# Kernel optimization log

Hardware: AMD Instinct MI355X
Metric: run time of the kernel (lower is better)

## Reference

```python
import jax, jax.numpy as jnp
import numpy as np

B, T_ENC, T_DEC, D, N_STATE = 32, 1024, 512, 512, 512


def setup_inputs() -> dict:
    key = jax.random.key(0)
    k1, k2, k3, k4 = jax.random.split(key, 4)
    scale = 1.0 / np.sqrt(D)
    return {
        "states_encoder": jax.random.normal(k1, (B, T_ENC, D), dtype=jnp.float32),
        "states_decoder": jax.random.normal(k2, (B, T_DEC, N_STATE), dtype=jnp.float32),
        "Wk": jax.random.normal(k3, (D, N_STATE), dtype=jnp.float32) * scale,
        "bk": jnp.zeros((N_STATE,), dtype=jnp.float32),
        "Wv": jax.random.normal(k4, (D, N_STATE), dtype=jnp.float32) * scale,
        "bv": jnp.zeros((N_STATE,), dtype=jnp.float32),
    }


def reference(states_encoder, states_decoder, Wk, bk, Wv, bv):
    # general Luong dot-product attention (n_state = int branch)
    key_vector = states_encoder @ Wk + bk          # [B, T_enc, N]
    val_vector = states_encoder @ Wv + bv          # [B, T_enc, N]
    # score[b, t_dec, t_enc] = sum_n dec[b,t_dec,n] * key[b,t_enc,n]
    score = jnp.einsum('bqn,bkn->bqk', states_decoder, key_vector)
    attention = jax.nn.softmax(score, axis=-1)     # over encoder positions
    # context[b, t_dec, n] = sum_k attention[b,t_dec,k] * val[b,k,n]
    context = jnp.einsum('bqk,bkn->bqn', attention, val_vector)
    return (context, attention)
```

## Files before the change

### kernel.cpp

```cpp
#include <hip/hip_runtime.h>
#include <math.h>

#define BB    32
#define TENC  1024
#define TDEC  512
#define DDIM  512
#define NST   512

typedef _Float16 f16_t;
typedef _Float16 f16x8 __attribute__((ext_vector_type(8)));
typedef _Float16 f16x4 __attribute__((ext_vector_type(4)));
typedef float    f32x4 __attribute__((ext_vector_type(4)));

#define GLOAD_LDS16(gp, lp) __builtin_amdgcn_global_load_lds( \
    (const __attribute__((address_space(1))) unsigned int*)(const void*)(gp), \
    (__attribute__((address_space(3))) unsigned int*)(lp), 16, 0, 0)

static __device__ __forceinline__ f32x4 MFMA16H(f16x8 a, f16x8 b, f32x4 c) {
    return __builtin_amdgcn_mfma_f32_16x16x32_f16(a, b, c, 0, 0, 0);
}

__global__ __launch_bounds__(256)
void prep_convert(const float* __restrict__ enc, const float* __restrict__ Wk,
                  const float* __restrict__ Wv,
                  f16_t* __restrict__ Ef16, f16_t* __restrict__ Wk16,
                  f16_t* __restrict__ WvT16)
{
    const int bid = blockIdx.x;
    const int t = threadIdx.x;

    if (bid < 8320) {
        const float* src; f16_t* dst; long i;
        if (bid < 8192) { src = enc; dst = Ef16; i = (long)bid * 256 + t; }
        else            { src = Wk;  dst = Wk16; i = (long)(bid - 8192) * 256 + t; }
        float4 a = *(const float4*)&src[i * 8];
        float4 b = *(const float4*)&src[i * 8 + 4];
        f16x8 o;
        o[0] = (f16_t)a.x; o[1] = (f16_t)a.y; o[2] = (f16_t)a.z; o[3] = (f16_t)a.w;
        o[4] = (f16_t)b.x; o[5] = (f16_t)b.y; o[6] = (f16_t)b.z; o[7] = (f16_t)b.w;
        *(f16x8*)&dst[i * 8] = o;
        return;
    }

    __shared__ f16_t tile[64][65];
    const int r2 = bid - 8320;
    const int c0 = (r2 & 7) * 64, r0 = (r2 >> 3) * 64;
    const int rr = t >> 4;
    const int cc = (t & 15) * 4;
#pragma unroll
    for (int p = 0; p < 4; ++p) {
        int r = rr + p * 16;
        float4 v = *(const float4*)&Wv[(long)(r0 + r) * NST + c0 + cc];
        tile[r][cc + 0] = (f16_t)v.x;
        tile[r][cc + 1] = (f16_t)v.y;
        tile[r][cc + 2] = (f16_t)v.z;
        tile[r][cc + 3] = (f16_t)v.w;
    }
    __syncthreads();
    const int dr = t >> 2;
    const int tc = (t & 3) * 16;
    f16_t tmp[16];
#pragma unroll
    for (int e = 0; e < 16; ++e) tmp[e] = tile[tc + e][dr];
    *(f16x8*)&WvT16[(long)(c0 + dr) * DDIM + r0 + tc]     = *(f16x8*)&tmp[0];
    *(f16x8*)&WvT16[(long)(c0 + dr) * DDIM + r0 + tc + 8] = *(f16x8*)&tmp[8];
}

__global__ __launch_bounds__(256)
void transpose_f16(const f16_t* __restrict__ in, f16_t* __restrict__ out,
                   int R, int C, long sIn, long sOut)
{
    __shared__ f16_t tile[64][65];
    const long b = blockIdx.z;
    in  += b * sIn;
    out += b * sOut;
    const int r0 = blockIdx.x * 64;
    const int c0 = blockIdx.y * 64;
    const int t = threadIdx.x;
    const int rr = t >> 4;
    const int cc = (t & 15) * 4;
#pragma unroll
    for (int p = 0; p < 4; ++p) {
        const int r = rr + p * 16;
        *(f16x4*)&tile[r][cc] = *(const f16x4*)&in[(long)(r0 + r) * C + c0 + cc];
    }
    __syncthreads();
    const int dr = t >> 2;
    const int tc = (t & 3) * 16;
    f16_t tmp[16];
#pragma unroll
    for (int e = 0; e < 16; ++e) tmp[e] = tile[tc + e][dr];
    *(f16x8*)&out[(long)(c0 + dr) * R + r0 + tc]     = *(f16x8*)&tmp[0];
    *(f16x8*)&out[(long)(c0 + dr) * R + r0 + tc + 8] = *(f16x8*)&tmp[8];
}

template<int EPI>
__global__ __launch_bounds__(256)
void gemm_h(const f16_t* __restrict__ A, const f16_t* __restrict__ B,
            void* __restrict__ C0,
            int M, int N, int K, long sA, long sB, long sC)
{
    __shared__ f16_t lds[2][8192];

    const int tid  = threadIdx.x;
    const int wave = tid >> 6;
    const int lane = tid & 63;

    const int gx = gridDim.x, gy = gridDim.y;
    const long nwg = (long)gx * gy * gridDim.z;
    const long fo  = ((long)blockIdx.z * gy + blockIdx.y) * gx + blockIdx.x;
    const long f2 = (fo & 7) * (nwg >> 3) + (fo >> 3);
    const int bx  = (int)(f2 % gx);
    const int by  = (int)((f2 / gx) % gy);
    const long bz = f2 / ((long)gx * gy);

    const f16_t* Ab = A + bz * sA;
    const f16_t* Bb = B + bz * sB;

    const int row0 = by * 128;
    const int col0 = bx * 128;

    const int srow  = wave * 16 + (lane >> 2);
    const int sslot = (lane & 3) ^ ((srow >> 1) & 3);
    const int wdst  = wave * 512;
    const long aOff0 = (long)(row0 + srow) * K + sslot * 8;
    const long aOff1 = (long)(row0 + 64 + srow) * K + sslot * 8;
    const long bOff0 = (long)(col0 + srow) * K + sslot * 8;
    const long bOff1 = (long)(col0 + 64 + srow) * K + sslot * 8;

    const int fr = lane & 15;
    const int q  = lane >> 4;
    const int wr = (wave >> 1) * 64;
    const int wc = (wave & 1) * 64;
    int aro[4], bro[4];
#pragma unroll
    for (int i = 0; i < 4; ++i) {
        const int r = wr + i * 16 + fr;
        aro[i] = r * 32 + ((q ^ ((r >> 1) & 3)) * 8);
    }
#pragma unroll
    for (int j = 0; j < 4; ++j) {
        const int r = wc + j * 16 + fr;
        bro[j] = r * 32 + ((q ^ ((r >> 1) & 3)) * 8);
    }

    f32x4 acc[4][4] = {};
    const int NT = K >> 5;

#define STAGE(buf, kt) do {                                   \
        GLOAD_LDS16(Ab + aOff0 + (kt), &(buf)[wdst]);         \
        GLOAD_LDS16(Ab + aOff1 + (kt), &(buf)[2048 + wdst]);  \
        GLOAD_LDS16(Bb + bOff0 + (kt), &(buf)[4096 + wdst]);  \
        GLOAD_LDS16(Bb + bOff1 + (kt), &(buf)[6144 + wdst]);  \
    } while (0)

    STAGE(lds[0], 0);

    for (int t = 0; t < NT; ++t) {
        const f16_t* cur = lds[t & 1];
        f16_t* nxt = lds[(t & 1) ^ 1];
        const bool pf = (t + 1 < NT);

        __builtin_amdgcn_sched_barrier(0);
        __builtin_amdgcn_s_barrier();
        if (pf) {
            STAGE(nxt, (t + 1) << 5);
            asm volatile("s_waitcnt vmcnt(4)" ::: "memory");
        } else {
            asm volatile("s_waitcnt vmcnt(0)" ::: "memory");
        }
        __builtin_amdgcn_s_barrier();
        __builtin_amdgcn_sched_barrier(0);

        f16x8 aH[4], bH[4];
#pragma unroll
        for (int i = 0; i < 4; ++i) aH[i] = *(const f16x8*)&cur[aro[i]];
#pragma unroll
        for (int j = 0; j < 4; ++j) bH[j] = *(const f16x8*)&cur[4096 + bro[j]];

#pragma unroll
        for (int j = 0; j < 4; ++j)
#pragma unroll
            for (int i = 0; i < 4; ++i)
                acc[i][j] = MFMA16H(aH[i], bH[j], acc[i][j]);
    }
#undef STAGE

    const int frow = q * 4;
#pragma unroll
    for (int i = 0; i < 4; ++i) {
        const int rgl = row0 + wr + i * 16 + frow;
#pragma unroll
        for (int j = 0; j < 4; ++j) {
            const int cg = col0 + wc + j * 16 + fr;
            if constexpr (EPI == 2) {
                f16_t* C = (f16_t*)C0 + bz * sC;
#pragma unroll
                for (int r = 0; r < 4; ++r)
                    C[(long)(rgl + r) * N + cg] = (f16_t)acc[i][j][r];
            } else {
                float* C = (float*)C0 + bz * sC;
#pragma unroll
                for (int r = 0; r < 4; ++r)
                    C[(long)(rgl + r) * N + cg] = acc[i][j][r];
            }
        }
    }
}

template<int EPI>
__global__ __launch_bounds__(256)
void gemm_rs(const float* __restrict__ Rf, const f16_t* __restrict__ Gh,
             const float* __restrict__ bias, void* __restrict__ C0,
             int M, int N, int K, long sRf, long sG, long sC)
{
    __shared__ f16_t lds[2][8192];

    const int tid  = threadIdx.x;
    const int wave = tid >> 6;
    const int lane = tid & 63;

    const int gx = gridDim.x, gy = gridDim.y;
    const long nwg = (long)gx * gy * gridDim.z;
    const long fo  = ((long)blockIdx.z * gy + blockIdx.y) * gx + blockIdx.x;
    const long f2 = (fo & 7) * (nwg >> 3) + (fo >> 3);
    const int bx  = (int)(f2 % gx);
    const int by  = (int)((f2 / gx) % gy);
    const long bz = f2 / ((long)gx * gy);

    const float* RfB = Rf + bz * sRf;
    const f16_t* GhB = Gh + bz * sG;

    const int row0 = by * 128;
    const int col0 = bx * 128;

    const int srow  = wave * 16 + (lane >> 2);
    const int sslot = (lane & 3) ^ ((srow >> 1) & 3);
    const int wdst  = wave * 512;

    const int rrow = tid >> 3;
    const int rk4  = (tid & 7) * 4;
    const int rgr  = rk4 >> 3;
    const int rh4  = rk4 & 4;

    const int fr = lane & 15;
    const int q  = lane >> 4;
    const int wr = (wave >> 1) * 64;
    const int wc = (wave & 1) * 64;
    int aro[4], bro[4];
#pragma unroll
    for (int i = 0; i < 4; ++i) {
        const int r = wr + i * 16 + fr;
        aro[i] = r * 32 + ((q ^ ((r >> 1) & 3)) * 8);
    }
#pragma unroll
    for (int j = 0; j < 4; ++j) {
        const int r = wc + j * 16 + fr;
        bro[j] = r * 32 + ((q ^ ((r >> 1) & 3)) * 8);
    }

    f32x4 acc[4][4] = {};
    float4 rS[4];
    f16x8 aH[4], bH[4];
    const int NT = K >> 5;

    auto stageG = [&](f16_t* buf, int kt) {
#pragma unroll
        for (int c = 0; c < 2; ++c) {
            const long go = (long)(col0 + c * 64 + srow) * K + kt + sslot * 8;
            GLOAD_LDS16(GhB + go, &buf[4096 + c * 2048 + wdst]);
        }
    };
    auto loadR = [&](int kt) {
#pragma unroll
        for (int i = 0; i < 4; ++i)
            rS[i] = *(const float4*)&RfB[(long)(row0 + i * 32 + rrow) * K + kt + rk4];
    };
    auto writeR = [&](f16_t* buf) {
#pragma unroll
        for (int i = 0; i < 4; ++i) {
            const int row = i * 32 + rrow;
            const int eo  = row * 32 + ((rgr ^ ((row >> 1) & 3)) * 8) + rh4;
            f16x4 h4;
            h4[0] = (f16_t)rS[i].x; h4[1] = (f16_t)rS[i].y;
            h4[2] = (f16_t)rS[i].z; h4[3] = (f16_t)rS[i].w;
            *(f16x4*)&buf[eo] = h4;
        }
    };
    auto readF = [&](const f16_t* buf) {
#pragma unroll
        for (int i = 0; i < 4; ++i) aH[i] = *(const f16x8*)&buf[aro[i]];
#pragma unroll
        for (int j = 0; j < 4; ++j) bH[j] = *(const f16x8*)&buf[4096 + bro[j]];
    };

    loadR(0);
    stageG(lds[0], 0);
    writeR(lds[0]);
    loadR(32);
    asm volatile("s_waitcnt vmcnt(4)" ::: "memory");
    asm volatile("s_waitcnt lgkmcnt(0)" ::: "memory");
    __builtin_amdgcn_s_barrier();
    readF(lds[0]);
    asm volatile("s_waitcnt lgkmcnt(0)" ::: "memory");
    __builtin_amdgcn_s_barrier();

    for (int t = 0; t < NT; ++t) {
        f16_t* nxt = lds[(t & 1) ^ 1];
        const bool pf = (t + 1 < NT);

        if (pf) {
            writeR(nxt);
            stageG(nxt, (t + 1) << 5);
            if (t + 2 < NT) loadR((t + 2) << 5);
        }
#pragma unroll
        for (int j = 0; j < 4; ++j)
#pragma unroll
            for (int i = 0; i < 4; ++i)
                acc[i][j] = MFMA16H(aH[i], bH[j], acc[i][j]);

        if (pf && (t + 2 < NT))
            asm volatile("s_waitcnt vmcnt(4)" ::: "memory");
        else
            asm volatile("s_waitcnt vmcnt(0)" ::: "memory");
        asm volatile("s_waitcnt lgkmcnt(0)" ::: "memory");
        __builtin_amdgcn_s_barrier();
        if (pf) {
            readF(nxt);
            asm volatile("s_waitcnt lgkmcnt(0)" ::: "memory");
        }
        __builtin_amdgcn_s_barrier();
    }

    const int frow = q * 4;
#pragma unroll
    for (int i = 0; i < 4; ++i) {
        const int rgl = row0 + wr + i * 16 + frow;
#pragma unroll
        for (int j = 0; j < 4; ++j) {
            const int cg = col0 + wc + j * 16 + fr;
            if constexpr (EPI == 2) {
                f16_t* C = (f16_t*)C0 + bz * sC;
#pragma unroll
                for (int r = 0; r < 4; ++r)
                    C[(long)(rgl + r) * N + cg] = (f16_t)acc[i][j][r];
            } else {
                float* C = (float*)C0 + bz * sC;
                const float badd = bias[cg];
#pragma unroll
                for (int r = 0; r < 4; ++r)
                    C[(long)(rgl + r) * N + cg] = acc[i][j][r] + badd;
            }
        }
    }
}

__global__ __launch_bounds__(256)
void softmax_rows(float* __restrict__ S)
{
    const long row = (long)blockIdx.x * 4 + (threadIdx.x >> 6);
    const int lane = threadIdx.x & 63;
    float* p = S + row * (long)TENC;

    float4 v[4];
    float m = -INFINITY;
#pragma unroll
    for (int i = 0; i < 4; ++i) {
        v[i] = *(const float4*)&p[i * 256 + lane * 4];
        m = fmaxf(fmaxf(fmaxf(v[i].x, v[i].y), fmaxf(v[i].z, v[i].w)), m);
    }
#pragma unroll
    for (int o = 32; o; o >>= 1) m = fmaxf(m, __shfl_xor(m, o, 64));

    float s = 0.f;
#pragma unroll
    for (int i = 0; i < 4; ++i) {
        v[i].x = __expf(v[i].x - m);
        v[i].y = __expf(v[i].y - m);
        v[i].z = __expf(v[i].z - m);
        v[i].w = __expf(v[i].w - m);
        s += v[i].x + v[i].y + v[i].z + v[i].w;
    }
#pragma unroll
    for (int o = 32; o; o >>= 1) s += __shfl_xor(s, o, 64);

    const float inv = 1.0f / s;
#pragma unroll
    for (int i = 0; i < 4; ++i) {
        v[i].x *= inv; v[i].y *= inv; v[i].z *= inv; v[i].w *= inv;
        *(float4*)&p[i * 256 + lane * 4] = v[i];
    }
}

#define TILE_M 64
#define TILE_N 64
#define TILE_K 16
template<bool B_TRANS, bool ADD_BIAS>
__global__ __launch_bounds__(256)
void gemm_f32(const float* __restrict__ A, const float* __restrict__ Bm,
              const float* __restrict__ bias, float* __restrict__ C,
              int M, int N, int K, int lda, int ldb,
              long strideA, long strideB, long strideC)
{
    __shared__ float As[TILE_K][TILE_M + 4];
    __shared__ float Bs[TILE_K][TILE_N + 4];
    const int b = blockIdx.z;
    A += (long)b * strideA; Bm += (long)b * strideB; C += (long)b * strideC;
    const int tid = threadIdx.x;
    const int tx = tid & 15, ty = tid >> 4;
    const int row0 = blockIdx.y * TILE_M, col0 = blockIdx.x * TILE_N;
    const int am = tid >> 2, ak = (tid & 3) * 4;
    float acc[4][4] = {};
    for (int kt = 0; kt < K; kt += TILE_K) {
        float4 a4 = *(const float4*)&A[(long)(row0 + am) * lda + kt + ak];
        float4 b4;
        if (B_TRANS) b4 = *(const float4*)&Bm[(long)(col0 + am) * ldb + kt + ak];
        else {
            const int bk_ = tid >> 4, bn = (tid & 15) * 4;
            b4 = *(const float4*)&Bm[(long)(kt + bk_) * ldb + col0 + bn];
        }
        __syncthreads();
        As[ak + 0][am] = a4.x; As[ak + 1][am] = a4.y;
        As[ak + 2][am] = a4.z; As[ak + 3][am] = a4.w;
        if (B_TRANS) {
            Bs[ak + 0][am] = b4.x; Bs[ak + 1][am] = b4.y;
            Bs[ak + 2][am] = b4.z; Bs[ak + 3][am] = b4.w;
        } else {
            const int bk_ = tid >> 4, bn = (tid & 15) * 4;
            *(float4*)&Bs[bk_][bn] = b4;
        }
        __syncthreads();
#pragma unroll
        for (int k = 0; k < TILE_K; ++k) {
            float4 av = *(const float4*)&As[k][ty * 4];
            float4 bv4 = *(const float4*)&Bs[k][tx * 4];
            float ar[4] = {av.x, av.y, av.z, av.w};
            float br[4] = {bv4.x, bv4.y, bv4.z, bv4.w};
#pragma unroll
            for (int i = 0; i < 4; ++i)
#pragma unroll
                for (int j = 0; j < 4; ++j)
                    acc[i][j] = fmaf(ar[i], br[j], acc[i][j]);
        }
    }
    float4 bias4 = make_float4(0.f, 0.f, 0.f, 0.f);
    if (ADD_BIAS) bias4 = *(const float4*)&bias[col0 + tx * 4];
#pragma unroll
    for (int i = 0; i < 4; ++i) {
        float4 o;
        o.x = acc[i][0] + bias4.x; o.y = acc[i][1] + bias4.y;
        o.z = acc[i][2] + bias4.z; o.w = acc[i][3] + bias4.w;
        *(float4*)&C[(long)(row0 + ty * 4 + i) * N + col0 + tx * 4] = o;
    }
}

extern "C" void kernel_launch(void* const* d_in, const int* in_sizes, int n_in,
                              void* d_out, int out_size, void* d_ws, size_t ws_size,
                              hipStream_t stream)
{
    const float* enc = (const float*)d_in[0];
    const float* dec = (const float*)d_in[1];
    const float* Wk  = (const float*)d_in[2];
    const float* Wv  = (const float*)d_in[4];
    const float* bv  = (const float*)d_in[5];

    const long nD = (long)BB * TDEC * NST;

    float* ctx   = (float*)d_out;
    float* attnF = ctx + nD;

    const size_t need = 68157440;
    const dim3 blk(256);

    if (ws_size < need) {
        float* ws = (float*)d_ws;
        gemm_f32<true, false><<<dim3(DDIM / 64, (BB * TDEC) / 64, 1), blk, 0, stream>>>(
            dec, Wk, nullptr, ws, BB * TDEC, DDIM, NST, NST, NST, 0, 0, 0);
        gemm_f32<true, false><<<dim3(TENC / 64, TDEC / 64, BB), blk, 0, stream>>>(
            ws, enc, nullptr, attnF, TDEC, TENC, DDIM, DDIM, DDIM,
            (long)TDEC * DDIM, (long)TENC * DDIM, (long)TDEC * TENC);
        softmax_rows<<<(BB * TDEC) / 4, blk, 0, stream>>>(attnF);
        gemm_f32<false, false><<<dim3(DDIM / 64, TDEC / 64, BB), blk, 0, stream>>>(
            attnF, enc, nullptr, ws, TDEC, DDIM, TENC, TENC, DDIM,
            (long)TDEC * TENC, (long)TENC * DDIM, (long)TDEC * DDIM);
        gemm_f32<false, true><<<dim3(NST / 64, (BB * TDEC) / 64, 1), blk, 0, stream>>>(
            ws, Wv, bv, ctx, BB * TDEC, NST, DDIM, DDIM, NST, 0, 0, 0);
        return;
    }

    char* w = (char*)d_ws;
    f16_t* EVT   = (f16_t*)(w);
    f16_t* Ef16  = (f16_t*)(w + 33554432);
    f16_t* Wk16  = (f16_t*)(w + 67108864);
    f16_t* WvT16 = (f16_t*)(w + 67633152);

    f16_t* DK16 = (f16_t*)ctx;
    f16_t* EV   = (f16_t*)attnF;

    prep_convert<<<8384, blk, 0, stream>>>(enc, Wk, Wv, Ef16, Wk16, WvT16);

    gemm_rs<2><<<dim3(DDIM / 128, (BB * TDEC) / 128, 1), blk, 0, stream>>>(
        dec, Wk16, nullptr, DK16,
        BB * TDEC, DDIM, NST, 0, 0, 0);

    gemm_h<2><<<dim3(NST / 128, (BB * TENC) / 128, 1), blk, 0, stream>>>(
        Ef16, WvT16, EV,
        BB * TENC, NST, DDIM, 0, 0, 0);

    transpose_f16<<<dim3(TENC / 64, NST / 64, BB), blk, 0, stream>>>(
        EV, EVT, TENC, NST, (long)TENC * NST, (long)NST * TENC);

    gemm_h<0><<<dim3(TENC / 128, TDEC / 128, BB), blk, 0, stream>>>(
        DK16, Ef16, attnF,
        TDEC, TENC, DDIM,
        (long)TDEC * DDIM, (long)TENC * DDIM, (long)TDEC * TENC);

    softmax_rows<<<(BB * TDEC) / 4, blk, 0, stream>>>(attnF);

    gemm_rs<3><<<dim3(NST / 128, TDEC / 128, BB), blk, 0, stream>>>(
        attnF, EVT, bv, ctx,
        TDEC, NST, TENC,
        (long)TDEC * TENC, (long)NST * TENC, (long)TDEC * NST);
}
```

Baseline: 173.5 us.

## Reassociate value projection after attention and read fp32 encoder directly in score GEMM

Instead of projecting encoder states through Wv and transposing the result, the pipeline now computes attention @ encoder and applies Wv (plus bias) afterwards on the smaller decoder-length output. The score GEMM reads the fp32 encoder directly through a register-staged path with a new AREG template switch, which removes the separate fp16 encoder conversion. A single fused convert-and-transpose of the encoder feeds the attention-times-encoder GEMM. This reduces total FLOPs and intermediate traffic because T_DEC is smaller than T_ENC. The cost is extra fp32 loads and in-kernel conversion in the score GEMM, plus an fp16 intermediate before the final projection.

```diff
diff --git a/kernel.cpp b/kernel.cpp
--- a/kernel.cpp
+++ b/kernel.cpp
@@ -21,29 +21,25 @@
 }
 
 __global__ __launch_bounds__(256)
-void prep_convert(const float* __restrict__ enc, const float* __restrict__ Wk,
-                  const float* __restrict__ Wv,
-                  f16_t* __restrict__ Ef16, f16_t* __restrict__ Wk16,
-                  f16_t* __restrict__ WvT16)
+void prep_weights(const float* __restrict__ Wk, const float* __restrict__ Wv,
+                  f16_t* __restrict__ Wk16, f16_t* __restrict__ WvT16)
 {
     const int bid = blockIdx.x;
     const int t = threadIdx.x;
 
-    if (bid < 8320) {
-        const float* src; f16_t* dst; long i;
-        if (bid < 8192) { src = enc; dst = Ef16; i = (long)bid * 256 + t; }
-        else            { src = Wk;  dst = Wk16; i = (long)(bid - 8192) * 256 + t; }
-        float4 a = *(const float4*)&src[i * 8];
-        float4 b = *(const float4*)&src[i * 8 + 4];
+    if (bid < 128) {
+        long i = (long)bid * 256 + t;
+        float4 a = *(const float4*)&Wk[i * 8];
+        float4 b = *(const float4*)&Wk[i * 8 + 4];
         f16x8 o;
         o[0] = (f16_t)a.x; o[1] = (f16_t)a.y; o[2] = (f16_t)a.z; o[3] = (f16_t)a.w;
         o[4] = (f16_t)b.x; o[5] = (f16_t)b.y; o[6] = (f16_t)b.z; o[7] = (f16_t)b.w;
-        *(f16x8*)&dst[i * 8] = o;
+        *(f16x8*)&Wk16[i * 8] = o;
         return;
     }
 
     __shared__ f16_t tile[64][65];
-    const int r2 = bid - 8320;
+    const int r2 = bid - 128;
     const int c0 = (r2 & 7) * 64, r0 = (r2 >> 3) * 64;
     const int rr = t >> 4;
     const int cc = (t & 15) * 4;
@@ -67,22 +63,25 @@
 }
 
 __global__ __launch_bounds__(256)
-void transpose_f16(const f16_t* __restrict__ in, f16_t* __restrict__ out,
-                   int R, int C, long sIn, long sOut)
+void transpose_ef(const float* __restrict__ in, f16_t* __restrict__ out)
 {
     __shared__ f16_t tile[64][65];
     const long b = blockIdx.z;
-    in  += b * sIn;
-    out += b * sOut;
-    const int r0 = blockIdx.x * 64;
-    const int c0 = blockIdx.y * 64;
+    const float* inB = in + b * (long)TENC * DDIM;
+    f16_t* outB = out + b * (long)DDIM * TENC;
+    const int te0 = blockIdx.x * 64;
+    const int d0  = blockIdx.y * 64;
     const int t = threadIdx.x;
     const int rr = t >> 4;
     const int cc = (t & 15) * 4;
 #pragma unroll
     for (int p = 0; p < 4; ++p) {
         const int r = rr + p * 16;
-        *(f16x4*)&tile[r][cc] = *(const f16x4*)&in[(long)(r0 + r) * C + c0 + cc];
+        float4 v = *(const float4*)&inB[(long)(te0 + r) * DDIM + d0 + cc];
+        tile[r][cc + 0] = (f16_t)v.x;
+        tile[r][cc + 1] = (f16_t)v.y;
+        tile[r][cc + 2] = (f16_t)v.z;
+        tile[r][cc + 3] = (f16_t)v.w;
     }
     __syncthreads();
     const int dr = t >> 2;
@@ -90,15 +89,15 @@
     f16_t tmp[16];
 #pragma unroll
     for (int e = 0; e < 16; ++e) tmp[e] = tile[tc + e][dr];
-    *(f16x8*)&out[(long)(c0 + dr) * R + r0 + tc]     = *(f16x8*)&tmp[0];
-    *(f16x8*)&out[(long)(c0 + dr) * R + r0 + tc + 8] = *(f16x8*)&tmp[8];
-}
-
-template<int EPI>
+    *(f16x8*)&outB[(long)(d0 + dr) * TENC + te0 + tc]     = *(f16x8*)&tmp[0];
+    *(f16x8*)&outB[(long)(d0 + dr) * TENC + te0 + tc + 8] = *(f16x8*)&tmp[8];
+}
+
+template<int AREG, int EPI>
 __global__ __launch_bounds__(256)
-void gemm_h(const f16_t* __restrict__ A, const f16_t* __restrict__ B,
-            void* __restrict__ C0,
-            int M, int N, int K, long sA, long sB, long sC)
+void gemm_rs(const float* __restrict__ Rf, const f16_t* __restrict__ Gh,
+             const float* __restrict__ bias, void* __restrict__ C0,
+             int M, int N, int K, long sRf, long sG, long sC)
 {
     __shared__ f16_t lds[2][8192];
 
@@ -114,19 +113,24 @@
     const int by  = (int)((f2 / gx) % gy);
     const long bz = f2 / ((long)gx * gy);
 
-    const f16_t* Ab = A + bz * sA;
-    const f16_t* Bb = B + bz * sB;
+    const float* RfB = Rf + bz * sRf;
+    const f16_t* GhB = Gh + bz * sG;
 
     const int row0 = by * 128;
     const int col0 = bx * 128;
+    const int rbase = AREG ? row0 : col0;
+    const int gbase = AREG ? col0 : row0;
+    constexpr int rOff = AREG ? 0 : 4096;
+    constexpr int gOff = AREG ? 4096 : 0;
 
     const int srow  = wave * 16 + (lane >> 2);
     const int sslot = (lane & 3) ^ ((srow >> 1) & 3);
     const int wdst  = wave * 512;
-    const long aOff0 = (long)(row0 + srow) * K + sslot * 8;
-    const long aOff1 = (long)(row0 + 64 + srow) * K + sslot * 8;
-    const long bOff0 = (long)(col0 + srow) * K + sslot * 8;
-    const long bOff1 = (long)(col0 + 64 + srow) * K + sslot * 8;
+
+    const int rrow = tid >> 3;
+    const int rk4  = (tid & 7) * 4;
+    const int rgr  = rk4 >> 3;
+    const int rh4  = rk4 & 4;
 
     const int fr = lane & 15;
     const int q  = lane >> 4;
@@ -145,121 +149,6 @@
     }
 
     f32x4 acc[4][4] = {};
-    const int NT = K >> 5;
-
-#define STAGE(buf, kt) do {                                   \
-        GLOAD_LDS16(Ab + aOff0 + (kt), &(buf)[wdst]);         \
-        GLOAD_LDS16(Ab + aOff1 + (kt), &(buf)[2048 + wdst]);  \
-        GLOAD_LDS16(Bb + bOff0 + (kt), &(buf)[4096 + wdst]);  \
-        GLOAD_LDS16(Bb + bOff1 + (kt), &(buf)[6144 + wdst]);  \
-    } while (0)
-
-    STAGE(lds[0], 0);
-
-    for (int t = 0; t < NT; ++t) {
-        const f16_t* cur = lds[t & 1];
-        f16_t* nxt = lds[(t & 1) ^ 1];
-        const bool pf = (t + 1 < NT);
-
-        __builtin_amdgcn_sched_barrier(0);
-        __builtin_amdgcn_s_barrier();
-        if (pf) {
-            STAGE(nxt, (t + 1) << 5);
-            asm volatile("s_waitcnt vmcnt(4)" ::: "memory");
-        } else {
-            asm volatile("s_waitcnt vmcnt(0)" ::: "memory");
-        }
-        __builtin_amdgcn_s_barrier();
-        __builtin_amdgcn_sched_barrier(0);
-
-        f16x8 aH[4], bH[4];
-#pragma unroll
-        for (int i = 0; i < 4; ++i) aH[i] = *(const f16x8*)&cur[aro[i]];
-#pragma unroll
-        for (int j = 0; j < 4; ++j) bH[j] = *(const f16x8*)&cur[4096 + bro[j]];
-
-#pragma unroll
-        for (int j = 0; j < 4; ++j)
-#pragma unroll
-            for (int i = 0; i < 4; ++i)
-                acc[i][j] = MFMA16H(aH[i], bH[j], acc[i][j]);
-    }
-#undef STAGE
-
-    const int frow = q * 4;
-#pragma unroll
-    for (int i = 0; i < 4; ++i) {
-        const int rgl = row0 + wr + i * 16 + frow;
-#pragma unroll
-        for (int j = 0; j < 4; ++j) {
-            const int cg = col0 + wc + j * 16 + fr;
-            if constexpr (EPI == 2) {
-                f16_t* C = (f16_t*)C0 + bz * sC;
-#pragma unroll
-                for (int r = 0; r < 4; ++r)
-                    C[(long)(rgl + r) * N + cg] = (f16_t)acc[i][j][r];
-            } else {
-                float* C = (float*)C0 + bz * sC;
-#pragma unroll
-                for (int r = 0; r < 4; ++r)
-                    C[(long)(rgl + r) * N + cg] = acc[i][j][r];
-            }
-        }
-    }
-}
-
-template<int EPI>
-__global__ __launch_bounds__(256)
-void gemm_rs(const float* __restrict__ Rf, const f16_t* __restrict__ Gh,
-             const float* __restrict__ bias, void* __restrict__ C0,
-             int M, int N, int K, long sRf, long sG, long sC)
-{
-    __shared__ f16_t lds[2][8192];
-
-    const int tid  = threadIdx.x;
-    const int wave = tid >> 6;
-    const int lane = tid & 63;
-
-    const int gx = gridDim.x, gy = gridDim.y;
-    const long nwg = (long)gx * gy * gridDim.z;
-    const long fo  = ((long)blockIdx.z * gy + blockIdx.y) * gx + blockIdx.x;
-    const long f2 = (fo & 7) * (nwg >> 3) + (fo >> 3);
-    const int bx  = (int)(f2 % gx);
-    const int by  = (int)((f2 / gx) % gy);
-    const long bz = f2 / ((long)gx * gy);
-
-    const float* RfB = Rf + bz * sRf;
-    const f16_t* GhB = Gh + bz * sG;
-
-    const int row0 = by * 128;
-    const int col0 = bx * 128;
-
-    const int srow  = wave * 16 + (lane >> 2);
-    const int sslot = (lane & 3) ^ ((srow >> 1) & 3);
-    const int wdst  = wave * 512;
-
-    const int rrow = tid >> 3;
-    const int rk4  = (tid & 7) * 4;
-    const int rgr  = rk4 >> 3;
-    const int rh4  = rk4 & 4;
-
-    const int fr = lane & 15;
-    const int q  = lane >> 4;
-    const int wr = (wave >> 1) * 64;
-    const int wc = (wave & 1) * 64;
-    int aro[4], bro[4];
-#pragma unroll
-    for (int i = 0; i < 4; ++i) {
-        const int r = wr + i * 16 + fr;
-        aro[i] = r * 32 + ((q ^ ((r >> 1) & 3)) * 8);
-    }
-#pragma unroll
-    for (int j = 0; j < 4; ++j) {
-        const int r = wc + j * 16 + fr;
-        bro[j] = r * 32 + ((q ^ ((r >> 1) & 3)) * 8);
-    }
-
-    f32x4 acc[4][4] = {};
     float4 rS[4];
     f16x8 aH[4], bH[4];
     const int NT = K >> 5;
@@ -267,14 +156,14 @@
     auto stageG = [&](f16_t* buf, int kt) {
 #pragma unroll
         for (int c = 0; c < 2; ++c) {
-            const long go = (long)(col0 + c * 64 + srow) * K + kt + sslot * 8;
-            GLOAD_LDS16(GhB + go, &buf[4096 + c * 2048 + wdst]);
+            const long go = (long)(gbase + c * 64 + srow) * K + kt + sslot * 8;
+            GLOAD_LDS16(GhB + go, &buf[gOff + c * 2048 + wdst]);
         }
     };
     auto loadR = [&](int kt) {
 #pragma unroll
         for (int i = 0; i < 4; ++i)
-            rS[i] = *(const float4*)&RfB[(long)(row0 + i * 32 + rrow) * K + kt + rk4];
+            rS[i] = *(const float4*)&RfB[(long)(rbase + i * 32 + rrow) * K + kt + rk4];
     };
     auto writeR = [&](f16_t* buf) {
 #pragma unroll
@@ -284,7 +173,7 @@
             f16x4 h4;
             h4[0] = (f16_t)rS[i].x; h4[1] = (f16_t)rS[i].y;
             h4[2] = (f16_t)rS[i].z; h4[3] = (f16_t)rS[i].w;
-            *(f16x4*)&buf[eo] = h4;
+            *(f16x4*)&buf[rOff + eo] = h4;
         }
     };
     auto readF = [&](const f16_t* buf) {
@@ -345,6 +234,131 @@
 #pragma unroll
                 for (int r = 0; r < 4; ++r)
                     C[(long)(rgl + r) * N + cg] = (f16_t)acc[i][j][r];
+            } else if constexpr (EPI == 0) {
+                float* C = (float*)C0 + bz * sC;
+#pragma unroll
+                for (int r = 0; r < 4; ++r)
+                    C[(long)(rgl + r) * N + cg] = acc[i][j][r];
+            } else {
+                float* C = (float*)C0 + bz * sC;
+                const float badd = bias[cg];
+#pragma unroll
+                for (int r = 0; r < 4; ++r)
+                    C[(long)(rgl + r) * N + cg] = acc[i][j][r] + badd;
+            }
+        }
+    }
+}
+
+template<int EPI>
+__global__ __launch_bounds__(256)
+void gemm_h(const f16_t* __restrict__ A, const f16_t* __restrict__ B,
+            const float* __restrict__ bias, void* __restrict__ C0,
+            int M, int N, int K, long sA, long sB, long sC)
+{
+    __shared__ f16_t lds[2][8192];
+
+    const int tid  = threadIdx.x;
+    const int wave = tid >> 6;
+    const int lane = tid & 63;
+
+    const int gx = gridDim.x, gy = gridDim.y;
+    const long nwg = (long)gx * gy * gridDim.z;
+    const long fo  = ((long)blockIdx.z * gy + blockIdx.y) * gx + blockIdx.x;
+    const long f2 = (fo & 7) * (nwg >> 3) + (fo >> 3);
+    const int bx  = (int)(f2 % gx);
+    const int by  = (int)((f2 / gx) % gy);
+    const long bz = f2 / ((long)gx * gy);
+
+    const f16_t* Ab = A + bz * sA;
+    const f16_t* Bb = B + bz * sB;
+
+    const int row0 = by * 128;
+    const int col0 = bx * 128;
+
+    const int srow  = wave * 16 + (lane >> 2);
+    const int sslot = (lane & 3) ^ ((srow >> 1) & 3);
+    const int wdst  = wave * 512;
+    const long aOff0 = (long)(row0 + srow) * K + sslot * 8;
+    const long aOff1 = (long)(row0 + 64 + srow) * K + sslot * 8;
+    const long bOff0 = (long)(col0 + srow) * K + sslot * 8;
+    const long bOff1 = (long)(col0 + 64 + srow) * K + sslot * 8;
+
+    const int fr = lane & 15;
+    const int q  = lane >> 4;
+    const int wr = (wave >> 1) * 64;
+    const int wc = (wave & 1) * 64;
+    int aro[4], bro[4];
+#pragma unroll
+    for (int i = 0; i < 4; ++i) {
+        const int r = wr + i * 16 + fr;
+        aro[i] = r * 32 + ((q ^ ((r >> 1) & 3)) * 8);
+    }
+#pragma unroll
+    for (int j = 0; j < 4; ++j) {
+        const int r = wc + j * 16 + fr;
+        bro[j] = r * 32 + ((q ^ ((r >> 1) & 3)) * 8);
+    }
+
+    f32x4 acc[4][4] = {};
+    const int NT = K >> 5;
+
+#define STAGE(buf, kt) do {                                   \
+        GLOAD_LDS16(Ab + aOff0 + (kt), &(buf)[wdst]);         \
+        GLOAD_LDS16(Ab + aOff1 + (kt), &(buf)[2048 + wdst]);  \
+        GLOAD_LDS16(Bb + bOff0 + (kt), &(buf)[4096 + wdst]);  \
+        GLOAD_LDS16(Bb + bOff1 + (kt), &(buf)[6144 + wdst]);  \
+    } while (0)
+
+    STAGE(lds[0], 0);
+
+    for (int t = 0; t < NT; ++t) {
+        const f16_t* cur = lds[t & 1];
+        f16_t* nxt = lds[(t & 1) ^ 1];
+        const bool pf = (t + 1 < NT);
+
+        __builtin_amdgcn_sched_barrier(0);
+        __builtin_amdgcn_s_barrier();
+        if (pf) {
+            STAGE(nxt, (t + 1) << 5);
+            asm volatile("s_waitcnt vmcnt(4)" ::: "memory");
+        } else {
+            asm volatile("s_waitcnt vmcnt(0)" ::: "memory");
+        }
+        __builtin_amdgcn_s_barrier();
+        __builtin_amdgcn_sched_barrier(0);
+
+        f16x8 aH[4], bH[4];
+#pragma unroll
+        for (int i = 0; i < 4; ++i) aH[i] = *(const f16x8*)&cur[aro[i]];
+#pragma unroll
+        for (int j = 0; j < 4; ++j) bH[j] = *(const f16x8*)&cur[4096 + bro[j]];
+
+#pragma unroll
+        for (int j = 0; j < 4; ++j)
+#pragma unroll
+            for (int i = 0; i < 4; ++i)
+                acc[i][j] = MFMA16H(aH[i], bH[j], acc[i][j]);
+    }
+#undef STAGE
+
+    const int frow = q * 4;
+#pragma unroll
+    for (int i = 0; i < 4; ++i) {
+        const int rgl = row0 + wr + i * 16 + frow;
+#pragma unroll
+        for (int j = 0; j < 4; ++j) {
+            const int cg = col0 + wc + j * 16 + fr;
+            if constexpr (EPI == 2) {
+                f16_t* C = (f16_t*)C0 + bz * sC;
+#pragma unroll
+                for (int r = 0; r < 4; ++r)
+                    C[(long)(rgl + r) * N + cg] = (f16_t)acc[i][j][r];
+            } else if constexpr (EPI == 0) {
+                float* C = (float*)C0 + bz * sC;
+#pragma unroll
+                for (int r = 0; r < 4; ++r)
+                    C[(long)(rgl + r) * N + cg] = acc[i][j][r];
             } else {
                 float* C = (float*)C0 + bz * sC;
                 const float badd = bias[cg];
@@ -470,7 +484,7 @@
     float* ctx   = (float*)d_out;
     float* attnF = ctx + nD;
 
-    const size_t need = 68157440;
+    const size_t need = 51380224;
     const dim3 blk(256);
 
     if (ws_size < need) {
@@ -490,36 +504,34 @@
     }
 
     char* w = (char*)d_ws;
-    f16_t* EVT   = (f16_t*)(w);
-    f16_t* Ef16  = (f16_t*)(w + 33554432);
-    f16_t* Wk16  = (f16_t*)(w + 67108864);
-    f16_t* WvT16 = (f16_t*)(w + 67633152);
+    f16_t* ET16  = (f16_t*)(w);
+    f16_t* AE16  = (f16_t*)(w + 33554432);
+    f16_t* Wk16  = (f16_t*)(w + 50331648);
+    f16_t* WvT16 = (f16_t*)(w + 50855936);
 
     f16_t* DK16 = (f16_t*)ctx;
-    f16_t* EV   = (f16_t*)attnF;
-
-    prep_convert<<<8384, blk, 0, stream>>>(enc, Wk, Wv, Ef16, Wk16, WvT16);
-
-    gemm_rs<2><<<dim3(DDIM / 128, (BB * TDEC) / 128, 1), blk, 0, stream>>>(
+
+    prep_weights<<<192, blk, 0, stream>>>(Wk, Wv, Wk16, WvT16);
+
+    transpose_ef<<<dim3(TENC / 64, DDIM / 64, BB), blk, 0, stream>>>(enc, ET16);
+
+    gemm_rs<1, 2><<<dim3(DDIM / 128, (BB * TDEC) / 128, 1), blk, 0, stream>>>(
         dec, Wk16, nullptr, DK16,
         BB * TDEC, DDIM, NST, 0, 0, 0);
 
-    gemm_h<2><<<dim3(NST / 128, (BB * TENC) / 128, 1), blk, 0, stream>>>(
-        Ef16, WvT16, EV,
-        BB * TENC, NST, DDIM, 0, 0, 0);
-
-    transpose_f16<<<dim3(TENC / 64, NST / 64, BB), blk, 0, stream>>>(
-        EV, EVT, TENC, NST, (long)TENC * NST, (long)NST * TENC);
-
-    gemm_h<0><<<dim3(TENC / 128, TDEC / 128, BB), blk, 0, stream>>>(
-        DK16, Ef16, attnF,
+    gemm_rs<0, 0><<<dim3(TENC / 128, TDEC / 128, BB), blk, 0, stream>>>(
+        enc, DK16, nullptr, attnF,
         TDEC, TENC, DDIM,
-        (long)TDEC * DDIM, (long)TENC * DDIM, (long)TDEC * TENC);
+        (long)TENC * DDIM, (long)TDEC * DDIM, (long)TDEC * TENC);
 
     softmax_rows<<<(BB * TDEC) / 4, blk, 0, stream>>>(attnF);
 
-    gemm_rs<3><<<dim3(NST / 128, TDEC / 128, BB), blk, 0, stream>>>(
-        attnF, EVT, bv, ctx,
-        TDEC, NST, TENC,
-        (long)TDEC * TENC, (long)NST * TENC, (long)TDEC * NST);
-}
+    gemm_rs<1, 2><<<dim3(DDIM / 128, TDEC / 128, BB), blk, 0, stream>>>(
+        attnF, ET16, nullptr, AE16,
+        TDEC, DDIM, TENC,
+        (long)TDEC * TENC, (long)DDIM * TENC, (long)TDEC * DDIM);
+
+    gemm_h<3><<<dim3(NST / 128, (BB * TDEC) / 128, 1), blk, 0, stream>>>(
+        AE16, WvT16, bv, ctx,
+        BB * TDEC, NST, DDIM, 0, 0, 0);
+}
```

Result: faster. 162.0 us (-6.6%).

## Compute transposed value projection directly and feed fp16 attention to final GEMM

Applied to the files above, without the earlier changes.

Drops the separate value-projection GEMM plus transpose kernel. The transposed values are now produced in a single batched GEMM, Wv^T times encoder^T, which writes EVT directly. Softmax also writes an fp16 copy of the attention into the no-longer-needed encoder fp16 buffer, so the final context GEMM can use the all-fp16 LDS-DMA gemm_h path instead of converting fp32 in registers. This removes one kernel launch and a full intermediate round trip through memory. In exchange, softmax writes an extra fp16 buffer and the buffer reuse depends on stream ordering.

```diff
diff --git a/kernel.cpp b/kernel.cpp
--- a/kernel.cpp
+++ b/kernel.cpp
@@ -66,39 +66,11 @@
     *(f16x8*)&WvT16[(long)(c0 + dr) * DDIM + r0 + tc + 8] = *(f16x8*)&tmp[8];
 }
 
+template<int AREG, int EPI>
 __global__ __launch_bounds__(256)
-void transpose_f16(const f16_t* __restrict__ in, f16_t* __restrict__ out,
-                   int R, int C, long sIn, long sOut)
-{
-    __shared__ f16_t tile[64][65];
-    const long b = blockIdx.z;
-    in  += b * sIn;
-    out += b * sOut;
-    const int r0 = blockIdx.x * 64;
-    const int c0 = blockIdx.y * 64;
-    const int t = threadIdx.x;
-    const int rr = t >> 4;
-    const int cc = (t & 15) * 4;
-#pragma unroll
-    for (int p = 0; p < 4; ++p) {
-        const int r = rr + p * 16;
-        *(f16x4*)&tile[r][cc] = *(const f16x4*)&in[(long)(r0 + r) * C + c0 + cc];
-    }
-    __syncthreads();
-    const int dr = t >> 2;
-    const int tc = (t & 3) * 16;
-    f16_t tmp[16];
-#pragma unroll
-    for (int e = 0; e < 16; ++e) tmp[e] = tile[tc + e][dr];
-    *(f16x8*)&out[(long)(c0 + dr) * R + r0 + tc]     = *(f16x8*)&tmp[0];
-    *(f16x8*)&out[(long)(c0 + dr) * R + r0 + tc + 8] = *(f16x8*)&tmp[8];
-}
-
-template<int EPI>
-__global__ __launch_bounds__(256)
-void gemm_h(const f16_t* __restrict__ A, const f16_t* __restrict__ B,
-            void* __restrict__ C0,
-            int M, int N, int K, long sA, long sB, long sC)
+void gemm_rs(const float* __restrict__ Rf, const f16_t* __restrict__ Gh,
+             const float* __restrict__ bias, void* __restrict__ C0,
+             int M, int N, int K, long sRf, long sG, long sC)
 {
     __shared__ f16_t lds[2][8192];
 
@@ -114,19 +86,24 @@
     const int by  = (int)((f2 / gx) % gy);
     const long bz = f2 / ((long)gx * gy);
 
-    const f16_t* Ab = A + bz * sA;
-    const f16_t* Bb = B + bz * sB;
+    const float* RfB = Rf + bz * sRf;
+    const f16_t* GhB = Gh + bz * sG;
 
     const int row0 = by * 128;
     const int col0 = bx * 128;
+    const int rbase = AREG ? row0 : col0;
+    const int gbase = AREG ? col0 : row0;
+    constexpr int rOff = AREG ? 0 : 4096;
+    constexpr int gOff = AREG ? 4096 : 0;
 
     const int srow  = wave * 16 + (lane >> 2);
     const int sslot = (lane & 3) ^ ((srow >> 1) & 3);
     const int wdst  = wave * 512;
-    const long aOff0 = (long)(row0 + srow) * K + sslot * 8;
-    const long aOff1 = (long)(row0 + 64 + srow) * K + sslot * 8;
-    const long bOff0 = (long)(col0 + srow) * K + sslot * 8;
-    const long bOff1 = (long)(col0 + 64 + srow) * K + sslot * 8;
+
+    const int rrow = tid >> 3;
+    const int rk4  = (tid & 7) * 4;
+    const int rgr  = rk4 >> 3;
+    const int rh4  = rk4 & 4;
 
     const int fr = lane & 15;
     const int q  = lane >> 4;
@@ -145,121 +122,6 @@
     }
 
     f32x4 acc[4][4] = {};
-    const int NT = K >> 5;
-
-#define STAGE(buf, kt) do {                                   \
-        GLOAD_LDS16(Ab + aOff0 + (kt), &(buf)[wdst]);         \
-        GLOAD_LDS16(Ab + aOff1 + (kt), &(buf)[2048 + wdst]);  \
-        GLOAD_LDS16(Bb + bOff0 + (kt), &(buf)[4096 + wdst]);  \
-        GLOAD_LDS16(Bb + bOff1 + (kt), &(buf)[6144 + wdst]);  \
-    } while (0)
-
-    STAGE(lds[0], 0);
-
-    for (int t = 0; t < NT; ++t) {
-        const f16_t* cur = lds[t & 1];
-        f16_t* nxt = lds[(t & 1) ^ 1];
-        const bool pf = (t + 1 < NT);
-
-        __builtin_amdgcn_sched_barrier(0);
-        __builtin_amdgcn_s_barrier();
-        if (pf) {
-            STAGE(nxt, (t + 1) << 5);
-            asm volatile("s_waitcnt vmcnt(4)" ::: "memory");
-        } else {
-            asm volatile("s_waitcnt vmcnt(0)" ::: "memory");
-        }
-        __builtin_amdgcn_s_barrier();
-        __builtin_amdgcn_sched_barrier(0);
-
-        f16x8 aH[4], bH[4];
-#pragma unroll
-        for (int i = 0; i < 4; ++i) aH[i] = *(const f16x8*)&cur[aro[i]];
-#pragma unroll
-        for (int j = 0; j < 4; ++j) bH[j] = *(const f16x8*)&cur[4096 + bro[j]];
-
-#pragma unroll
-        for (int j = 0; j < 4; ++j)
-#pragma unroll
-            for (int i = 0; i < 4; ++i)
-                acc[i][j] = MFMA16H(aH[i], bH[j], acc[i][j]);
-    }
-#undef STAGE
-
-    const int frow = q * 4;
-#pragma unroll
-    for (int i = 0; i < 4; ++i) {
-        const int rgl = row0 + wr + i * 16 + frow;
-#pragma unroll
-        for (int j = 0; j < 4; ++j) {
-            const int cg = col0 + wc + j * 16 + fr;
-            if constexpr (EPI == 2) {
-                f16_t* C = (f16_t*)C0 + bz * sC;
-#pragma unroll
-                for (int r = 0; r < 4; ++r)
-                    C[(long)(rgl + r) * N + cg] = (f16_t)acc[i][j][r];
-            } else {
-                float* C = (float*)C0 + bz * sC;
-#pragma unroll
-                for (int r = 0; r < 4; ++r)
-                    C[(long)(rgl + r) * N + cg] = acc[i][j][r];
-            }
-        }
-    }
-}
-
-template<int EPI>
-__global__ __launch_bounds__(256)
-void gemm_rs(const float* __restrict__ Rf, const f16_t* __restrict__ Gh,
-             const float* __restrict__ bias, void* __restrict__ C0,
-             int M, int N, int K, long sRf, long sG, long sC)
-{
-    __shared__ f16_t lds[2][8192];
-
-    const int tid  = threadIdx.x;
-    const int wave = tid >> 6;
-    const int lane = tid & 63;
-
-    const int gx = gridDim.x, gy = gridDim.y;
-    const long nwg = (long)gx * gy * gridDim.z;
-    const long fo  = ((long)blockIdx.z * gy + blockIdx.y) * gx + blockIdx.x;
-    const long f2 = (fo & 7) * (nwg >> 3) + (fo >> 3);
-    const int bx  = (int)(f2 % gx);
-    const int by  = (int)((f2 / gx) % gy);
-    const long bz = f2 / ((long)gx * gy);
-
-    const float* RfB = Rf + bz * sRf;
-    const f16_t* GhB = Gh + bz * sG;
-
-    const int row0 = by * 128;
-    const int col0 = bx * 128;
-
-    const int srow  = wave * 16 + (lane >> 2);
-    const int sslot = (lane & 3) ^ ((srow >> 1) & 3);
-    const int wdst  = wave * 512;
-
-    const int rrow = tid >> 3;
-    const int rk4  = (tid & 7) * 4;
-    const int rgr  = rk4 >> 3;
-    const int rh4  = rk4 & 4;
-
-    const int fr = lane & 15;
-    const int q  = lane >> 4;
-    const int wr = (wave >> 1) * 64;
-    const int wc = (wave & 1) * 64;
-    int aro[4], bro[4];
-#pragma unroll
-    for (int i = 0; i < 4; ++i) {
-        const int r = wr + i * 16 + fr;
-        aro[i] = r * 32 + ((q ^ ((r >> 1) & 3)) * 8);
-    }
-#pragma unroll
-    for (int j = 0; j < 4; ++j) {
-        const int r = wc + j * 16 + fr;
-        bro[j] = r * 32 + ((q ^ ((r >> 1) & 3)) * 8);
-    }
-
-    f32x4 acc[4][4] = {};
     float4 rS[4];
     f16x8 aH[4], bH[4];
     const int NT = K >> 5;
@@ -267,14 +129,14 @@
     auto stageG = [&](f16_t* buf, int kt) {
 #pragma unroll
         for (int c = 0; c < 2; ++c) {
-            const long go = (long)(col0 + c * 64 + srow) * K + kt + sslot * 8;
-            GLOAD_LDS16(GhB + go, &buf[4096 + c * 2048 + wdst]);
+            const long go = (long)(gbase + c * 64 + srow) * K + kt + sslot * 8;
+            GLOAD_LDS16(GhB + go, &buf[gOff + c * 2048 + wdst]);
         }
     };
     auto loadR = [&](int kt) {
 #pragma unroll
         for (int i = 0; i < 4; ++i)
-            rS[i] = *(const float4*)&RfB[(long)(row0 + i * 32 + rrow) * K + kt + rk4];
+            rS[i] = *(const float4*)&RfB[(long)(rbase + i * 32 + rrow) * K + kt + rk4];
     };
     auto writeR = [&](f16_t* buf) {
 #pragma unroll
@@ -284,7 +146,7 @@
             f16x4 h4;
             h4[0] = (f16_t)rS[i].x; h4[1] = (f16_t)rS[i].y;
             h4[2] = (f16_t)rS[i].z; h4[3] = (f16_t)rS[i].w;
-            *(f16x4*)&buf[eo] = h4;
+            *(f16x4*)&buf[rOff + eo] = h4;
         }
     };
     auto readF = [&](const f16_t* buf) {
@@ -345,6 +207,11 @@
 #pragma unroll
                 for (int r = 0; r < 4; ++r)
                     C[(long)(rgl + r) * N + cg] = (f16_t)acc[i][j][r];
+            } else if constexpr (EPI == 0) {
+                float* C = (float*)C0 + bz * sC;
+#pragma unroll
+                for (int r = 0; r < 4; ++r)
+                    C[(long)(rgl + r) * N + cg] = acc[i][j][r];
             } else {
                 float* C = (float*)C0 + bz * sC;
                 const float badd = bias[cg];
@@ -356,8 +223,128 @@
     }
 }
 
+template<int EPI>
 __global__ __launch_bounds__(256)
-void softmax_rows(float* __restrict__ S)
+void gemm_h(const f16_t* __restrict__ A, const f16_t* __restrict__ B,
+            const float* __restrict__ bias, void* __restrict__ C0,
+            int M, int N, int K, long sA, long sB, long sC)
+{
+    __shared__ f16_t lds[2][8192];
+
+    const int tid  = threadIdx.x;
+    const int wave = tid >> 6;
+    const int lane = tid & 63;
+
+    const int gx = gridDim.x, gy = gridDim.y;
+    const long nwg = (long)gx * gy * gridDim.z;
+    const long fo  = ((long)blockIdx.z * gy + blockIdx.y) * gx + blockIdx.x;
+    const long f2 = (fo & 7) * (nwg >> 3) + (fo >> 3);
+    const int bx  = (int)(f2 % gx);
+    const int by  = (int)((f2 / gx) % gy);
+    const long bz = f2 / ((long)gx * gy);
+
+    const f16_t* Ab = A + bz * sA;
+    const f16_t* Bb = B + bz * sB;
+
+    const int row0 = by * 128;
+    const int col0 = bx * 128;
+
+    const int srow  = wave * 16 + (lane >> 2);
+    const int sslot = (lane & 3) ^ ((srow >> 1) & 3);
+    const int wdst  = wave * 512;
+    const long aOff0 = (long)(row0 + srow) * K + sslot * 8;
+    const long aOff1 = (long)(row0 + 64 + srow) * K + sslot * 8;
+    const long bOff0 = (long)(col0 + srow) * K + sslot * 8;
+    const long bOff1 = (long)(col0 + 64 + srow) * K + sslot * 8;
+
+    const int fr = lane & 15;
+    const int q  = lane >> 4;
+    const int wr = (wave >> 1) * 64;
+    const int wc = (wave & 1) * 64;
+    int aro[4], bro[4];
+#pragma unroll
+    for (int i = 0; i < 4; ++i) {
+        const int r = wr + i * 16 + fr;
+        aro[i] = r * 32 + ((q ^ ((r >> 1) & 3)) * 8);
+    }
+#pragma unroll
+    for (int j = 0; j < 4; ++j) {
+        const int r = wc + j * 16 + fr;
+        bro[j] = r * 32 + ((q ^ ((r >> 1) & 3)) * 8);
+    }
+
+    f32x4 acc[4][4] = {};
+    const int NT = K >> 5;
+
+#define STAGE(buf, kt) do {                                   \
+        GLOAD_LDS16(Ab + aOff0 + (kt), &(buf)[wdst]);         \
+        GLOAD_LDS16(Ab + aOff1 + (kt), &(buf)[2048 + wdst]);  \
+        GLOAD_LDS16(Bb + bOff0 + (kt), &(buf)[4096 + wdst]);  \
+        GLOAD_LDS16(Bb + bOff1 + (kt), &(buf)[6144 + wdst]);  \
+    } while (0)
+
+    STAGE(lds[0], 0);
+
+    for (int t = 0; t < NT; ++t) {
+        const f16_t* cur = lds[t & 1];
+        f16_t* nxt = lds[(t & 1) ^ 1];
+        const bool pf = (t + 1 < NT);
+
+        __builtin_amdgcn_sched_barrier(0);
+        __builtin_amdgcn_s_barrier();
+        if (pf) {
+            STAGE(nxt, (t + 1) << 5);
+            asm volatile("s_waitcnt vmcnt(4)" ::: "memory");
+        } else {
+            asm volatile("s_waitcnt vmcnt(0)" ::: "memory");
+        }
+        __builtin_amdgcn_s_barrier();
+        __builtin_amdgcn_sched_barrier(0);
+
+        f16x8 aH[4], bH[4];
+#pragma unroll
+        for (int i = 0; i < 4; ++i) aH[i] = *(const f16x8*)&cur[aro[i]];
+#pragma unroll
+        for (int j = 0; j < 4; ++j) bH[j] = *(const f16x8*)&cur[4096 + bro[j]];
+
+#pragma unroll
+        for (int j = 0; j < 4; ++j)
+#pragma unroll
+            for (int i = 0; i < 4; ++i)
+                acc[i][j] = MFMA16H(aH[i], bH[j], acc[i][j]);
+    }
+#undef STAGE
+
+    const int frow = q * 4;
+#pragma unroll
+    for (int i = 0; i < 4; ++i) {
+        const int rgl = row0 + wr + i * 16 + frow;
+#pragma unroll
+        for (int j = 0; j < 4; ++j) {
+            const int cg = col0 + wc + j * 16 + fr;
+            if constexpr (EPI == 2) {
+                f16_t* C = (f16_t*)C0 + bz * sC;
+#pragma unroll
+                for (int r = 0; r < 4; ++r)
+                    C[(long)(rgl + r) * N + cg] = (f16_t)acc[i][j][r];
+            } else if constexpr (EPI == 0) {
+                float* C = (float*)C0 + bz * sC;
+#pragma unroll
+                for (int r = 0; r < 4; ++r)
+                    C[(long)(rgl + r) * N + cg] = acc[i][j][r];
+            } else {
+                float* C = (float*)C0 + bz * sC;
+                const float badd = bias[cg];
+#pragma unroll
+                for (int r = 0; r < 4; ++r)
+                    C[(long)(rgl + r) * N + cg] = acc[i][j][r] + badd;
+            }
+        }
+    }
+}
+
+__global__ __launch_bounds__(256)
+void softmax_rows(float* __restrict__ S, f16_t* __restrict__ Sh)
 {
     const long row = (long)blockIdx.x * 4 + (threadIdx.x >> 6);
     const int lane = threadIdx.x & 63;
@@ -390,6 +377,12 @@
     for (int i = 0; i < 4; ++i) {
         v[i].x *= inv; v[i].y *= inv; v[i].z *= inv; v[i].w *= inv;
         *(float4*)&p[i * 256 + lane * 4] = v[i];
+        if (Sh) {
+            f16x4 h;
+            h[0] = (f16_t)v[i].x; h[1] = (f16_t)v[i].y;
+            h[2] = (f16_t)v[i].z; h[3] = (f16_t)v[i].w;
+            *(f16x4*)&Sh[row * (long)TENC + i * 256 + lane * 4] = h;
+        }
     }
 }
 
@@ -480,7 +473,7 @@
         gemm_f32<true, false><<<dim3(TENC / 64, TDEC / 64, BB), blk, 0, stream>>>(
             ws, enc, nullptr, attnF, TDEC, TENC, DDIM, DDIM, DDIM,
             (long)TDEC * DDIM, (long)TENC * DDIM, (long)TDEC * TENC);
-        softmax_rows<<<(BB * TDEC) / 4, blk, 0, stream>>>(attnF);
+        softmax_rows<<<(BB * TDEC) / 4, blk, 0, stream>>>(attnF, nullptr);
         gemm_f32<false, false><<<dim3(DDIM / 64, TDEC / 64, BB), blk, 0, stream>>>(
             attnF, enc, nullptr, ws, TDEC, DDIM, TENC, TENC, DDIM,
             (long)TDEC * TENC, (long)TENC * DDIM, (long)TDEC * DDIM);
@@ -494,32 +487,30 @@
     f16_t* Ef16  = (f16_t*)(w + 33554432);
     f16_t* Wk16  = (f16_t*)(w + 67108864);
     f16_t* WvT16 = (f16_t*)(w + 67633152);
+    f16_t* attnB = Ef16;
 
     f16_t* DK16 = (f16_t*)ctx;
-    f16_t* EV   = (f16_t*)attnF;
 
     prep_convert<<<8384, blk, 0, stream>>>(enc, Wk, Wv, Ef16, Wk16, WvT16);
 
-    gemm_rs<2><<<dim3(DDIM / 128, (BB * TDEC) / 128, 1), blk, 0, stream>>>(
+    gemm_rs<1, 2><<<dim3(DDIM / 128, (BB * TDEC) / 128, 1), blk, 0, stream>>>(
         dec, Wk16, nullptr, DK16,
         BB * TDEC, DDIM, NST, 0, 0, 0);
 
-    gemm_h<2><<<dim3(NST / 128, (BB * TENC) / 128, 1), blk, 0, stream>>>(
-        Ef16, WvT16, EV,
-        BB * TENC, NST, DDIM, 0, 0, 0);
-
-    transpose_f16<<<dim3(TENC / 64, NST / 64, BB), blk, 0, stream>>>(
-        EV, EVT, TENC, NST, (long)TENC * NST, (long)NST * TENC);
-
     gemm_h<0><<<dim3(TENC / 128, TDEC / 128, BB), blk, 0, stream>>>(
-        DK16, Ef16, attnF,
+        DK16, Ef16, nullptr, attnF,
         TDEC, TENC, DDIM,
         (long)TDEC * DDIM, (long)TENC * DDIM, (long)TDEC * TENC);
 
-    softmax_rows<<<(BB * TDEC) / 4, blk, 0, stream>>>(attnF);
-
-    gemm_rs<3><<<dim3(NST / 128, TDEC / 128, BB), blk, 0, stream>>>(
-        attnF, EVT, bv, ctx,
+    gemm_h<2><<<dim3(TENC / 128, NST / 128, BB), blk, 0, stream>>>(
+        WvT16, Ef16, nullptr, EVT,
+        NST, TENC, DDIM,
+        0, (long)TENC * DDIM, (long)NST * TENC);
+
+    softmax_rows<<<(BB * TDEC) / 4, blk, 0, stream>>>(attnF, attnB);
+
+    gemm_h<3><<<dim3(NST / 128, TDEC / 128, BB), blk, 0, stream>>>(
+        attnB, EVT, bv, ctx,
         TDEC, NST, TENC,
         (long)TDEC * TENC, (long)NST * TENC, (long)TDEC * NST);
 }
```

New measurement: 152.8 us (median of 2 runs). -12.0%, faster.
